# Performance work log

Measured on AMD Instinct MI355X. Metric: run time of the kernel, lower is better.

The kernel has to match this reference:

```python
import jax, jax.numpy as jnp
import numpy as np

TEMP = 0.3

def setup_inputs() -> dict:
    key = jax.random.key(0)
    k1, k2, k3 = jax.random.split(key, 3)
    N, d, T, Q = 2048, 256, 256, 64
    scale = 1.0 / np.sqrt(d)  # keep dot/temp in a numerically safe range for exp
    x = jax.random.normal(k1, (N, d), jnp.float32) * scale
    y = jax.random.normal(k2, (T, Q, d), jnp.float32) * scale
    track_idxs = jax.random.randint(k3, (N,), 0, T, dtype=jnp.int32)
    return {"x": x, "track_idxs": track_idxs, "y": y}


def reference(x, track_idxs, y):
    # Defaults: global_contrast=True, separate_tracks=True, static_contrast=True,
    # soft_condition=True, sim_type='dot'. Vectorized segment-sum form of the
    # per-unique-track Python loop in the original module.
    T, Q, d = y.shape
    yf = y.reshape(T * Q, d)                       # flatten(0,1): track-major
    y_idxs = jnp.tile(jnp.arange(T, dtype=jnp.int32), Q)  # torch .repeat(Q) == tile
    tid = track_idxs.astype(jnp.int32)

    S_xy = jnp.exp(x @ yf.T / TEMP)                # [N, T*Q]
    S_xx = jnp.exp(x @ x.T / TEMP)                 # [N, N]

    # Sum S columns grouped by (buggy-but-faithful) y track id / x track id -> [N, T]
    xy_by_track = jax.ops.segment_sum(S_xy.T, y_idxs, num_segments=T).T
    xx_by_track = jax.ops.segment_sum(S_xx.T, tid, num_segments=T).T

    rxy_total = S_xy.sum(axis=1)                   # [N]
    rxx_total = S_xx.sum(axis=1)                   # [N]
    rxy_pos = jnp.take_along_axis(xy_by_track, tid[:, None], axis=1)[:, 0]
    rxx_pos_full = jnp.take_along_axis(xx_by_track, tid[:, None], axis=1)[:, 0]
    rxx_pos = rxx_pos_full - jnp.diagonal(S_xx)    # exclude self-pairs (1 - eye)

    # per-row numerator/denominator contributions
    num_i = rxy_pos + 0.5 * rxx_pos                # static same-track sum halved
    den_i = (rxy_total - rxy_pos) + (rxx_total - rxx_pos_full)

    num_t = jax.ops.segment_sum(num_i, tid, num_segments=T)  # [T]
    den_t = jax.ops.segment_sum(den_i, tid, num_segments=T)
    counts = jax.ops.segment_sum(jnp.ones_like(num_i), tid, num_segments=T)
    present = counts > 0                            # unique() track ids

    num_safe = jnp.where(present, num_t, 1.0)
    den_safe = jnp.where(present, den_t, 0.0)
    loss_t = -jnp.log(num_safe / (den_safe + num_safe))  # soft_condition loss
    loss_t = jnp.where(present, loss_t, 0.0)
    n_present = present.sum().astype(loss_t.dtype)
    return (loss_t.sum() / n_present).reshape(1)
```

## Files before the change

kernel.cpp:

```cpp
#include <hip/hip_runtime.h>
#include <hip/hip_bf16.h>

#define NN   2048
#define DD   256
#define TT   256
#define NYC  16384
#define NCHUNK_XY 64
#define NCHUNK_XX 8
#define CHUNK_COLS 256
#define PAIR_BYTES 1040
#define TILE_BYTES (8 * PAIR_BYTES)

static constexpr float INV_TEMP = 1.0f / 0.3f;

typedef __bf16 bf16x8 __attribute__((ext_vector_type(8)));
typedef __bf16 bf16x4 __attribute__((ext_vector_type(4)));
typedef float  f32x4  __attribute__((ext_vector_type(4)));

__global__ void cvt_zero_kernel(const float* __restrict__ x, const float* __restrict__ y,
                                __bf16* __restrict__ xbf, __bf16* __restrict__ ybf,
                                float* __restrict__ acc ) {
    const int tid0   = blockIdx.x * blockDim.x + threadIdx.x;
    const int stride = gridDim.x * blockDim.x;
    for (int j = tid0; j < 3 * NN; j += stride) acc[j] = 0.f;
    const int nx4 = NN * DD / 4;
    const float4* x4 = (const float4*)x;
    for (int j = tid0; j < nx4; j += stride) {
        float4 v = x4[j];
        bf16x4 o; o[0] = (__bf16)v.x; o[1] = (__bf16)v.y; o[2] = (__bf16)v.z; o[3] = (__bf16)v.w;
        *(bf16x4*)(xbf + 4 * (size_t)j) = o;
    }
    const int ny4 = NYC * DD / 4;
    const float4* y4 = (const float4*)y;
    for (int j = tid0; j < ny4; j += stride) {
        float4 v = y4[j];
        bf16x4 o; o[0] = (__bf16)v.x; o[1] = (__bf16)v.y; o[2] = (__bf16)v.z; o[3] = (__bf16)v.w;
        *(bf16x4*)(ybf + 4 * (size_t)j) = o;
    }
}

__global__ void stats_kernel(const __bf16* __restrict__ xbf, const __bf16* __restrict__ ybf,
                             const int* __restrict__ tid,
                             float* __restrict__ Tot, float* __restrict__ Pxy,
                             float* __restrict__ Pxx, float* __restrict__ diag) {
    __shared__ __align__(16) char bstage[2][TILE_BYTES];
    __shared__ int coltid_s[CHUNK_COLS];

    const int tix  = threadIdx.x;
    const int w    = tix >> 6;
    const int lane = tix & 63;
    const int c16  = lane & 15;
    const int q    = lane >> 4;
    const int rowbase = blockIdx.x * 128 + w * 32;

    const int by    = blockIdx.y;
    const int mode  = (by >= NCHUNK_XY);
    const int chunk = mode ? (by - NCHUNK_XY) : by;
    const int colbase = chunk * CHUNK_COLS;
    const __bf16* colmat = mode ? xbf : ybf;

    coltid_s[tix] = mode ? tid[colbase + tix] : ((colbase + tix) & (TT - 1));

    bf16x8 afrag[2][8];
#pragma unroll
    for (int t = 0; t < 2; t++) {
        const __bf16* base = xbf + (size_t)(rowbase + t * 16 + c16) * DD + q * 8;
#pragma unroll
        for (int ks = 0; ks < 8; ks++)
            afrag[t][ks] = *(const bf16x8*)(base + ks * 32);
    }
    int tidrow[2][4];
#pragma unroll
    for (int t = 0; t < 2; t++)
#pragma unroll
        for (int r = 0; r < 4; r++)
            tidrow[t][r] = tid[rowbase + t * 16 + q * 4 + r];

    const int pair = tix >> 5;
    const int poff = (tix * 32) & 1023;
    char* dst0 = &bstage[0][pair * PAIR_BYTES + poff];
    char* dst1 = &bstage[1][pair * PAIR_BYTES + poff];

    float4 pf0, pf1;
    {
        const __bf16* src = colmat + (size_t)colbase * DD + tix * 16;
        pf0 = *(const float4*)src;
        pf1 = *(const float4*)(src + 8);
    }

    float tot[2][4] = {}, pos[2][4] = {};

    for (int ct = 0; ct < CHUNK_COLS / 16; ct++) {
        char* dst = (ct & 1) ? dst1 : dst0;
        *(float4*)dst        = pf0;
        *(float4*)(dst + 16) = pf1;
        if (ct < 15) {
            const __bf16* src = colmat + (size_t)(colbase + (ct + 1) * 16) * DD + tix * 16;
            pf0 = *(const float4*)src;
            pf1 = *(const float4*)(src + 8);
        }
        __syncthreads();

        const char* bb = &bstage[ct & 1][(c16 >> 1) * PAIR_BYTES + (c16 & 1) * 512 + q * 16];
        f32x4 acc0 = {0.f, 0.f, 0.f, 0.f};
        f32x4 acc1 = {0.f, 0.f, 0.f, 0.f};
#pragma unroll
        for (int ks = 0; ks < 8; ks++) {
            bf16x8 b = *(const bf16x8*)(bb + ks * 64);
            acc0 = __builtin_amdgcn_mfma_f32_16x16x32_bf16(afrag[0][ks], b, acc0, 0, 0, 0);
            acc1 = __builtin_amdgcn_mfma_f32_16x16x32_bf16(afrag[1][ks], b, acc1, 0, 0, 0);
        }

        const int colg   = colbase + ct * 16 + c16;
        const int coltid = coltid_s[ct * 16 + c16];
#pragma unroll
        for (int t = 0; t < 2; t++) {
            f32x4 acc = t ? acc1 : acc0;
#pragma unroll
            for (int r = 0; r < 4; r++) {
                float val = __expf(acc[r] * INV_TEMP);
                tot[t][r] += val;
                pos[t][r] += (coltid == tidrow[t][r]) ? val : 0.f;
                if (mode && colg == rowbase + t * 16 + q * 4 + r)
                    diag[colg] = val;
            }
        }
    }

#pragma unroll
    for (int t = 0; t < 2; t++)
#pragma unroll
        for (int r = 0; r < 4; r++) {
            float a = tot[t][r], p = pos[t][r];
#pragma unroll
            for (int off = 1; off < 16; off <<= 1) {
                a += __shfl_xor(a, off);
                p += __shfl_xor(p, off);
            }
            if (c16 == 0) {
                const int row = rowbase + t * 16 + q * 4 + r;
                atomicAdd(&Tot[row], a);
                atomicAdd(mode ? &Pxx[row] : &Pxy[row], p);
            }
        }
}

__global__ void finalize_kernel(const float* __restrict__ Tot, const float* __restrict__ Pxy,
                                const float* __restrict__ Pxx, const float* __restrict__ diag,
                                const int* __restrict__ tid, float* __restrict__ out) {
    __shared__ float num_s[TT], den_s[TT];
    __shared__ int cnt_s[TT];
    const int t = threadIdx.x;
    num_s[t] = 0.f; den_s[t] = 0.f; cnt_s[t] = 0;
    __syncthreads();
    for (int i = t; i < NN; i += 256) {
        float tt_ = Tot[i], pxy = Pxy[i], pxx = Pxx[i];
        float num = pxy + 0.5f * (pxx - diag[i]);
        float den = tt_ - pxy - pxx;
        int tr = tid[i];
        atomicAdd(&num_s[tr], num);
        atomicAdd(&den_s[tr], den);
        atomicAdd(&cnt_s[tr], 1);
    }
    __syncthreads();
    float lt = 0.f, pr = 0.f;
    if (cnt_s[t] > 0) {
        lt = -logf(num_s[t] / (den_s[t] + num_s[t]));
        pr = 1.f;
    }
    for (int off = 32; off; off >>= 1) { lt += __shfl_down(lt, off); pr += __shfl_down(pr, off); }
    __shared__ float ls[4], ps[4];
    if ((t & 63) == 0) { ls[t >> 6] = lt; ps[t >> 6] = pr; }
    __syncthreads();
    if (t == 0) out[0] = (ls[0] + ls[1] + ls[2] + ls[3]) / (ps[0] + ps[1] + ps[2] + ps[3]);
}

extern "C" void kernel_launch(void* const* d_in, const int* in_sizes, int n_in,
                              void* d_out, int out_size, void* d_ws, size_t ws_size,
                              hipStream_t stream) {
    const float* x   = (const float*)d_in[0];
    const int*   tid = (const int*)d_in[1];
    const float* y   = (const float*)d_in[2];
    float* out = (float*)d_out;

    char* ws = (char*)d_ws;
    __bf16* xbf = (__bf16*)ws;
    __bf16* ybf = (__bf16*)(ws + (1u << 20));
    float* acc  = (float*)(ws + 9u * (1u << 20));
    float* Tot  = acc;
    float* Pxy  = acc + NN;
    float* Pxx  = acc + 2 * NN;
    float* diag = acc + 3 * NN;

    cvt_zero_kernel<<<1024, 256, 0, stream>>>(x, y, xbf, ybf, acc);
    stats_kernel<<<dim3(16, NCHUNK_XY + NCHUNK_XX), 256, 0, stream>>>(
        xbf, ybf, tid, Tot, Pxy, Pxx, diag);
    finalize_kernel<<<1, 256, 0, stream>>>(Tot, Pxy, Pxx, diag, tid, out);
}
```

Measured before the change: 114.4 us.

## Pre-swizzle column operands into MFMA fragment layout and drop LDS staging

The prep kernel now writes y and x columns into one buffer already arranged in MFMA B-fragment order. The stats kernel can then load B operands straight from global memory into registers, double-buffered across column tiles, with no LDS staging or __syncthreads. The diagonal of S_xx moves into the prep kernel as exp of the bf16-rounded row norm, which removes the per-element diagonal check from the epilogue. In exchange, prep writes an extra copy of x, the column tid is read from global memory in each epilogue, and register pressure rises from holding two B fragment sets.

```diff
diff --git a/kernel.cpp b/kernel.cpp
--- a/kernel.cpp
+++ b/kernel.cpp
@@ -5,11 +5,11 @@
 #define DD   256
 #define TT   256
 #define NYC  16384
+#define NCOLS (NYC + NN)
 #define NCHUNK_XY 64
 #define NCHUNK_XX 8
-#define CHUNK_COLS 256
-#define PAIR_BYTES 1040
-#define TILE_BYTES (8 * PAIR_BYTES)
+#define NCHUNKS (NCHUNK_XY + NCHUNK_XX)
+#define NFRAG (NCOLS / 16 * 8 * 64)
 
 static constexpr float INV_TEMP = 1.0f / 0.3f;
 
@@ -17,49 +17,60 @@
 typedef __bf16 bf16x4 __attribute__((ext_vector_type(4)));
 typedef float  f32x4  __attribute__((ext_vector_type(4)));
 
-__global__ void cvt_zero_kernel(const float* __restrict__ x, const float* __restrict__ y,
-                                __bf16* __restrict__ xbf, __bf16* __restrict__ ybf,
-                                float* __restrict__ acc ) {
-    const int tid0   = blockIdx.x * blockDim.x + threadIdx.x;
-    const int stride = gridDim.x * blockDim.x;
-    for (int j = tid0; j < 3 * NN; j += stride) acc[j] = 0.f;
-    const int nx4 = NN * DD / 4;
-    const float4* x4 = (const float4*)x;
-    for (int j = tid0; j < nx4; j += stride) {
-        float4 v = x4[j];
+__device__ __forceinline__ float bfr(float v) { return (float)(__bf16)v; }
+
+__global__ void prep_kernel(const float* __restrict__ x, const float* __restrict__ y,
+                            __bf16* __restrict__ xbf, __bf16* __restrict__ cols,
+                            float* __restrict__ acc, float* __restrict__ diag) {
+    const int t0 = blockIdx.x * 256 + threadIdx.x;
+
+    if (t0 < 3 * NN) acc[t0] = 0.f;
+
+    if (t0 < NN * 8) {
+        const int row = t0 >> 3, sub = t0 & 7;
+        const float4* xr = (const float4*)(x + (size_t)row * DD) + sub * 8;
+        float s = 0.f;
+#pragma unroll
+        for (int u = 0; u < 8; u++) {
+            float4 v = xr[u];
+            float a = bfr(v.x), b = bfr(v.y), c = bfr(v.z), d = bfr(v.w);
+            s += a * a + b * b + c * c + d * d;
+        }
+        s += __shfl_xor(s, 1); s += __shfl_xor(s, 2); s += __shfl_xor(s, 4);
+        if (sub == 0) diag[row] = __expf(s * INV_TEMP);
+    }
+
+    if (t0 < NN * DD / 4) {
+        float4 v = ((const float4*)x)[t0];
         bf16x4 o; o[0] = (__bf16)v.x; o[1] = (__bf16)v.y; o[2] = (__bf16)v.z; o[3] = (__bf16)v.w;
-        *(bf16x4*)(xbf + 4 * (size_t)j) = o;
-    }
-    const int ny4 = NYC * DD / 4;
-    const float4* y4 = (const float4*)y;
-    for (int j = tid0; j < ny4; j += stride) {
-        float4 v = y4[j];
-        bf16x4 o; o[0] = (__bf16)v.x; o[1] = (__bf16)v.y; o[2] = (__bf16)v.z; o[3] = (__bf16)v.w;
-        *(bf16x4*)(ybf + 4 * (size_t)j) = o;
-    }
-}
-
-__global__ void stats_kernel(const __bf16* __restrict__ xbf, const __bf16* __restrict__ ybf,
+        *(bf16x4*)(xbf + 4 * (size_t)t0) = o;
+    }
+
+    for (int f = t0; f < NFRAG; f += 262144) {
+        const int lane = f & 63, ks = (f >> 6) & 7, g = f >> 9;
+        const int col  = g * 16 + (lane & 15);
+        const int koff = ks * 32 + (lane >> 4) * 8;
+        const float* src = (col < NYC ? y + (size_t)col * DD
+                                      : x + (size_t)(col - NYC) * DD) + koff;
+        float4 v0 = *(const float4*)src, v1 = *(const float4*)(src + 4);
+        bf16x8 o;
+        o[0] = (__bf16)v0.x; o[1] = (__bf16)v0.y; o[2] = (__bf16)v0.z; o[3] = (__bf16)v0.w;
+        o[4] = (__bf16)v1.x; o[5] = (__bf16)v1.y; o[6] = (__bf16)v1.z; o[7] = (__bf16)v1.w;
+        *(bf16x8*)(cols + (size_t)f * 8) = o;
+    }
+}
+
+__global__ void stats_kernel(const __bf16* __restrict__ xbf, const __bf16* __restrict__ cols,
                              const int* __restrict__ tid,
                              float* __restrict__ Tot, float* __restrict__ Pxy,
-                             float* __restrict__ Pxx, float* __restrict__ diag) {
-    __shared__ __align__(16) char bstage[2][TILE_BYTES];
-    __shared__ int coltid_s[CHUNK_COLS];
-
-    const int tix  = threadIdx.x;
-    const int w    = tix >> 6;
-    const int lane = tix & 63;
+                             float* __restrict__ Pxx) {
+    const int w    = threadIdx.x >> 6;
+    const int lane = threadIdx.x & 63;
     const int c16  = lane & 15;
     const int q    = lane >> 4;
     const int rowbase = blockIdx.x * 128 + w * 32;
-
-    const int by    = blockIdx.y;
-    const int mode  = (by >= NCHUNK_XY);
-    const int chunk = mode ? (by - NCHUNK_XY) : by;
-    const int colbase = chunk * CHUNK_COLS;
-    const __bf16* colmat = mode ? xbf : ybf;
-
-    coltid_s[tix] = mode ? tid[colbase + tix] : ((colbase + tix) & (TT - 1));
+    const int chunk   = blockIdx.y;
+    const int mode    = (chunk >= NCHUNK_XY);
 
     bf16x8 afrag[2][8];
 #pragma unroll
@@ -76,55 +87,56 @@
         for (int r = 0; r < 4; r++)
             tidrow[t][r] = tid[rowbase + t * 16 + q * 4 + r];
 
-    const int pair = tix >> 5;
-    const int poff = (tix * 32) & 1023;
-    char* dst0 = &bstage[0][pair * PAIR_BYTES + poff];
-    char* dst1 = &bstage[1][pair * PAIR_BYTES + poff];
-
-    float4 pf0, pf1;
-    {
-        const __bf16* src = colmat + (size_t)colbase * DD + tix * 16;
-        pf0 = *(const float4*)src;
-        pf1 = *(const float4*)(src + 8);
-    }
-
     float tot[2][4] = {}, pos[2][4] = {};
 
-    for (int ct = 0; ct < CHUNK_COLS / 16; ct++) {
-        char* dst = (ct & 1) ? dst1 : dst0;
-        *(float4*)dst        = pf0;
-        *(float4*)(dst + 16) = pf1;
-        if (ct < 15) {
-            const __bf16* src = colmat + (size_t)(colbase + (ct + 1) * 16) * DD + tix * 16;
-            pf0 = *(const float4*)src;
-            pf1 = *(const float4*)(src + 8);
-        }
-        __syncthreads();
-
-        const char* bb = &bstage[ct & 1][(c16 >> 1) * PAIR_BYTES + (c16 & 1) * 512 + q * 16];
-        f32x4 acc0 = {0.f, 0.f, 0.f, 0.f};
-        f32x4 acc1 = {0.f, 0.f, 0.f, 0.f};
-#pragma unroll
-        for (int ks = 0; ks < 8; ks++) {
-            bf16x8 b = *(const bf16x8*)(bb + ks * 64);
-            acc0 = __builtin_amdgcn_mfma_f32_16x16x32_bf16(afrag[0][ks], b, acc0, 0, 0, 0);
-            acc1 = __builtin_amdgcn_mfma_f32_16x16x32_bf16(afrag[1][ks], b, acc1, 0, 0, 0);
-        }
-
-        const int colg   = colbase + ct * 16 + c16;
-        const int coltid = coltid_s[ct * 16 + c16];
+    const __bf16* fb = cols + ((size_t)chunk * 16 * 512 + lane) * 8;
+
+    bf16x8 b0[8], b1[8];
+#pragma unroll
+    for (int ks = 0; ks < 8; ks++) b0[ks] = *(const bf16x8*)(fb + ks * 512);
+
+    auto epilogue = [&](const f32x4& a0, const f32x4& a1, int ct) {
+        int coltid;
+        if (!mode) coltid = ct * 16 + c16;
+        else       coltid = tid[(chunk - NCHUNK_XY) * 256 + ct * 16 + c16];
 #pragma unroll
         for (int t = 0; t < 2; t++) {
-            f32x4 acc = t ? acc1 : acc0;
+            const f32x4& a = t ? a1 : a0;
 #pragma unroll
             for (int r = 0; r < 4; r++) {
-                float val = __expf(acc[r] * INV_TEMP);
+                float val = __expf(a[r] * INV_TEMP);
                 tot[t][r] += val;
                 pos[t][r] += (coltid == tidrow[t][r]) ? val : 0.f;
-                if (mode && colg == rowbase + t * 16 + q * 4 + r)
-                    diag[colg] = val;
             }
         }
+    };
+
+    for (int ct = 0; ct < 16; ct += 2) {
+        {
+            const __bf16* nb = fb + (size_t)(ct + 1) * 4096;
+#pragma unroll
+            for (int ks = 0; ks < 8; ks++) b1[ks] = *(const bf16x8*)(nb + ks * 512);
+        }
+        f32x4 acc0 = {0.f, 0.f, 0.f, 0.f}, acc1 = {0.f, 0.f, 0.f, 0.f};
+#pragma unroll
+        for (int ks = 0; ks < 8; ks++) {
+            acc0 = __builtin_amdgcn_mfma_f32_16x16x32_bf16(afrag[0][ks], b0[ks], acc0, 0, 0, 0);
+            acc1 = __builtin_amdgcn_mfma_f32_16x16x32_bf16(afrag[1][ks], b0[ks], acc1, 0, 0, 0);
+        }
+        epilogue(acc0, acc1, ct);
+
+        if (ct + 2 < 16) {
+            const __bf16* nb = fb + (size_t)(ct + 2) * 4096;
+#pragma unroll
+            for (int ks = 0; ks < 8; ks++) b0[ks] = *(const bf16x8*)(nb + ks * 512);
+        }
+        acc0 = (f32x4){0.f, 0.f, 0.f, 0.f}; acc1 = (f32x4){0.f, 0.f, 0.f, 0.f};
+#pragma unroll
+        for (int ks = 0; ks < 8; ks++) {
+            acc0 = __builtin_amdgcn_mfma_f32_16x16x32_bf16(afrag[0][ks], b1[ks], acc0, 0, 0, 0);
+            acc1 = __builtin_amdgcn_mfma_f32_16x16x32_bf16(afrag[1][ks], b1[ks], acc1, 0, 0, 0);
+        }
+        epilogue(acc0, acc1, ct + 1);
     }
 
 #pragma unroll
@@ -184,16 +196,15 @@
     float* out = (float*)d_out;
 
     char* ws = (char*)d_ws;
-    __bf16* xbf = (__bf16*)ws;
-    __bf16* ybf = (__bf16*)(ws + (1u << 20));
-    float* acc  = (float*)(ws + 9u * (1u << 20));
-    float* Tot  = acc;
-    float* Pxy  = acc + NN;
-    float* Pxx  = acc + 2 * NN;
-    float* diag = acc + 3 * NN;
-
-    cvt_zero_kernel<<<1024, 256, 0, stream>>>(x, y, xbf, ybf, acc);
-    stats_kernel<<<dim3(16, NCHUNK_XY + NCHUNK_XX), 256, 0, stream>>>(
-        xbf, ybf, tid, Tot, Pxy, Pxx, diag);
+    __bf16* xbf  = (__bf16*)ws;
+    __bf16* cols = (__bf16*)(ws + (1u << 20));
+    float* acc   = (float*)(ws + 11u * (1u << 20));
+    float* Tot   = acc;
+    float* Pxy   = acc + NN;
+    float* Pxx   = acc + 2 * NN;
+    float* diag  = acc + 3 * NN;
+
+    prep_kernel<<<1024, 256, 0, stream>>>(x, y, xbf, cols, acc, diag);
+    stats_kernel<<<dim3(16, NCHUNKS), 256, 0, stream>>>(xbf, cols, tid, Tot, Pxy, Pxx);
     finalize_kernel<<<1, 256, 0, stream>>>(Tot, Pxy, Pxx, diag, tid, out);
 }
```

Result: slower. 263.3 us (+130.1%).
